# Kernel optimization log

Measured on AMD Instinct MI355X. Metric: run time of the kernel, lower is better.

The kernel has to match this reference:

```python
import jax, jax.numpy as jnp
import numpy as np

EMB, HID, VOCAB, N_SUB = 1024, 2048, 50257, 64
T = N_SUB * 4  # 256 sequential decode steps


def setup_inputs() -> dict:
    key = jax.random.key(0)
    ks = jax.random.split(key, 7)
    s = 0.02  # small init to keep gates out of saturation, like trained weights
    return {
        "emb": jax.random.normal(ks[0], (VOCAB, EMB), jnp.float32) * s,
        "W_ih": jax.random.normal(ks[1], (4 * HID, EMB), jnp.float32) * s,
        "W_hh": jax.random.normal(ks[2], (4 * HID, HID), jnp.float32) * s,
        "b_ih": jax.random.normal(ks[3], (4 * HID,), jnp.float32) * s,
        "b_hh": jax.random.normal(ks[4], (4 * HID,), jnp.float32) * s,
        "W_out": jax.random.normal(ks[5], (VOCAB, HID), jnp.float32) * s,
        "b_out": jax.random.normal(ks[6], (VOCAB,), jnp.float32) * s,
    }


def reference(emb, W_ih, W_hh, b_ih, b_hh, W_out, b_out):
    H = W_hh.shape[1]

    def step(carry, _):
        tok, h, c = carry
        x = emb[tok]  # [EMB] embedding lookup of current token
        # PyTorch LSTM gate order: i, f, g, o
        gates = x @ W_ih.T + b_ih + h @ W_hh.T + b_hh  # [4H]
        i, f, g, o = jnp.split(gates, 4)
        i = jax.nn.sigmoid(i)
        f = jax.nn.sigmoid(f)
        g = jnp.tanh(g)
        o = jax.nn.sigmoid(o)
        c = f * c + i * g
        h = o * jnp.tanh(c)
        logits = h @ W_out.T + b_out  # [VOCAB]
        tok = jnp.argmax(logits).astype(jnp.int32)  # greedy feedback
        return (tok, h, c), logits

    init = (jnp.int32(0), jnp.zeros((H,), emb.dtype), jnp.zeros((H,), emb.dtype))
    _, logits = jax.lax.scan(step, init, None, length=T)
    return logits  # [T, VOCAB] == torch.cat(tokens, 0).squeeze()
```

## Files before the change

### kernel.cpp

```cpp
#include <hip/hip_runtime.h>

#define EMB    1024
#define HID    2048
#define VOCAB  50257
#define T      256
#define NB_LOG 1024
#define NB_GAT (HID / 4)
#define NB_CVT 2048

#define NEG_INF (-3.402823466e38f)


__global__ void k_init(float* __restrict__ ws) {
    int i = blockIdx.x * blockDim.x + threadIdx.x;
    if (i < 3 * HID) ws[i] = 0.0f;
}

__device__ __forceinline__ ushort f2bf(float f) {
    uint32_t u = __float_as_uint(f);
    u += 0x7FFFu + ((u >> 16) & 1u);
    return (ushort)(u >> 16);
}

__global__ __launch_bounds__(256) void k_cvt(const float* __restrict__ src,
                                             ushort* __restrict__ dst, int n4) {
    const int stride = gridDim.x * blockDim.x;
    for (int i = blockIdx.x * blockDim.x + threadIdx.x; i < n4; i += stride) {
        float4 v = ((const float4*)src)[i];
        ushort4 o;
        o.x = f2bf(v.x); o.y = f2bf(v.y); o.z = f2bf(v.z); o.w = f2bf(v.w);
        ((ushort4*)dst)[i] = o;
    }
}

__global__ __launch_bounds__(256) void k_gates(
    const float* __restrict__ emb,
    const float* __restrict__ W_ih, const float* __restrict__ W_hh,
    const float* __restrict__ b_ih, const float* __restrict__ b_hh,
    const float* __restrict__ h_in, float* __restrict__ h_out,
    float* __restrict__ c,
    const float* __restrict__ bmax, const int* __restrict__ bidx,
    int step)
{
    __shared__ float xs[EMB];
    __shared__ float hs[HID];
    __shared__ float redv[4];
    __shared__ int   redi[4];
    __shared__ int   tok_s;

    const int tid  = threadIdx.x;
    const int wave = tid >> 6;
    const int lane = tid & 63;

    if (step == 0) {
        if (tid == 0) tok_s = 0;
    } else {
        float bv = NEG_INF; int bi = 0x7fffffff;
        for (int i = tid; i < NB_LOG; i += 256) {
            float v = bmax[i]; int ix = bidx[i];
            if (v > bv || (v == bv && ix < bi)) { bv = v; bi = ix; }
        }
        for (int off = 32; off; off >>= 1) {
            float ov = __shfl_down(bv, off);
            int   oi = __shfl_down(bi, off);
            if (ov > bv || (ov == bv && oi < bi)) { bv = ov; bi = oi; }
        }
        if (lane == 0) { redv[wave] = bv; redi[wave] = bi; }
        __syncthreads();
        if (tid == 0) {
            for (int w = 1; w < 4; ++w)
                if (redv[w] > bv || (redv[w] == bv && redi[w] < bi)) { bv = redv[w]; bi = redi[w]; }
            tok_s = bi;
        }
    }
    __syncthreads();
    const int tok = tok_s;

    const float* xrow = emb + (size_t)tok * EMB;
    for (int i = tid; i < EMB; i += 256) xs[i] = xrow[i];
    for (int i = tid; i < HID; i += 256) hs[i] = h_in[i];
    __syncthreads();

    const int j = blockIdx.x * 4 + wave;
    float gv[4];
    #pragma unroll
    for (int g = 0; g < 4; ++g) {
        const int row = g * HID + j;
        const float* wi = W_ih + (size_t)row * EMB;
        const float* wh = W_hh + (size_t)row * HID;
        float acc = 0.0f;
        #pragma unroll
        for (int k = lane * 4; k < EMB; k += 256) {
            float4 w4 = *(const float4*)(wi + k);
            float4 x4 = *(const float4*)(xs + k);
            acc += w4.x * x4.x + w4.y * x4.y + w4.z * x4.z + w4.w * x4.w;
        }
        #pragma unroll
        for (int k = lane * 4; k < HID; k += 256) {
            float4 w4 = *(const float4*)(wh + k);
            float4 h4 = *(const float4*)(hs + k);
            acc += w4.x * h4.x + w4.y * h4.y + w4.z * h4.z + w4.w * h4.w;
        }
        for (int off = 32; off; off >>= 1) acc += __shfl_down(acc, off);
        gv[g] = acc;
    }

    if (lane == 0) {
        float gi = gv[0] + b_ih[j]           + b_hh[j];
        float gf = gv[1] + b_ih[HID + j]     + b_hh[HID + j];
        float gg = gv[2] + b_ih[2 * HID + j] + b_hh[2 * HID + j];
        float go = gv[3] + b_ih[3 * HID + j] + b_hh[3 * HID + j];
        float iv = 1.0f / (1.0f + expf(-gi));
        float fv = 1.0f / (1.0f + expf(-gf));
        float gvv = tanhf(gg);
        float ov = 1.0f / (1.0f + expf(-go));
        float cn = fv * c[j] + iv * gvv;
        c[j] = cn;
        h_out[j] = ov * tanhf(cn);
    }
}

__global__ __launch_bounds__(256) void k_logits_bf16(
    const ushort* __restrict__ Wb, const float* __restrict__ b_out,
    const float* __restrict__ h, float* __restrict__ out,
    float* __restrict__ bmax, int* __restrict__ bidx, int step)
{
    __shared__ float hs[HID];
    __shared__ float redv[4];
    __shared__ int   redi[4];

    const int tid  = threadIdx.x;
    const int wave = tid >> 6;
    const int lane = tid & 63;

    for (int i = tid; i < HID; i += 256) hs[i] = h[i];
    __syncthreads();

    float* orow = out + (size_t)step * VOCAB;
    float bv = NEG_INF; int bi = 0x7fffffff;

    for (int r = blockIdx.x * 4 + wave; r < VOCAB; r += NB_LOG * 4) {
        const ushort* w = Wb + (size_t)r * HID;
        float acc = 0.0f;
        #pragma unroll
        for (int k = lane * 4; k < HID; k += 256) {
            uint2 wv = *(const uint2*)(w + k);
            float4 h4 = *(const float4*)(hs + k);
            float w0 = __uint_as_float(wv.x << 16);
            float w1 = __uint_as_float(wv.x & 0xFFFF0000u);
            float w2 = __uint_as_float(wv.y << 16);
            float w3 = __uint_as_float(wv.y & 0xFFFF0000u);
            acc += w0 * h4.x + w1 * h4.y + w2 * h4.z + w3 * h4.w;
        }
        for (int off = 32; off; off >>= 1) acc += __shfl_down(acc, off);
        if (lane == 0) {
            float v = acc + b_out[r];
            orow[r] = v;
            if (v > bv) { bv = v; bi = r; }
        }
    }

    if (lane == 0) { redv[wave] = bv; redi[wave] = bi; }
    __syncthreads();
    if (tid == 0) {
        for (int w = 1; w < 4; ++w)
            if (redv[w] > bv || (redv[w] == bv && redi[w] < bi)) { bv = redv[w]; bi = redi[w]; }
        bmax[blockIdx.x] = bv;
        bidx[blockIdx.x] = bi;
    }
}

__global__ __launch_bounds__(256) void k_logits(
    const float* __restrict__ W_out, const float* __restrict__ b_out,
    const float* __restrict__ h, float* __restrict__ out,
    float* __restrict__ bmax, int* __restrict__ bidx, int step)
{
    __shared__ float hs[HID];
    __shared__ float redv[4];
    __shared__ int   redi[4];

    const int tid  = threadIdx.x;
    const int wave = tid >> 6;
    const int lane = tid & 63;

    for (int i = tid; i < HID; i += 256) hs[i] = h[i];
    __syncthreads();

    float* orow = out + (size_t)step * VOCAB;
    float bv = NEG_INF; int bi = 0x7fffffff;

    for (int r = blockIdx.x * 4 + wave; r < VOCAB; r += NB_LOG * 4) {
        const float* w = W_out + (size_t)r * HID;
        float acc = 0.0f;
        #pragma unroll
        for (int k = lane * 4; k < HID; k += 256) {
            float4 w4 = *(const float4*)(w + k);
            float4 h4 = *(const float4*)(hs + k);
            acc += w4.x * h4.x + w4.y * h4.y + w4.z * h4.z + w4.w * h4.w;
        }
        for (int off = 32; off; off >>= 1) acc += __shfl_down(acc, off);
        if (lane == 0) {
            float v = acc + b_out[r];
            orow[r] = v;
            if (v > bv) { bv = v; bi = r; }
        }
    }

    if (lane == 0) { redv[wave] = bv; redi[wave] = bi; }
    __syncthreads();
    if (tid == 0) {
        for (int w = 1; w < 4; ++w)
            if (redv[w] > bv || (redv[w] == bv && redi[w] < bi)) { bv = redv[w]; bi = redi[w]; }
        bmax[blockIdx.x] = bv;
        bidx[blockIdx.x] = bi;
    }
}

extern "C" void kernel_launch(void* const* d_in, const int* in_sizes, int n_in,
                              void* d_out, int out_size, void* d_ws, size_t ws_size,
                              hipStream_t stream) {
    const float* emb   = (const float*)d_in[0];
    const float* W_ih  = (const float*)d_in[1];
    const float* W_hh  = (const float*)d_in[2];
    const float* b_ih  = (const float*)d_in[3];
    const float* b_hh  = (const float*)d_in[4];
    const float* W_out = (const float*)d_in[5];
    const float* b_out = (const float*)d_in[6];
    float* out = (float*)d_out;

    float* ws   = (float*)d_ws;
    float* hA   = ws;
    float* hB   = ws + HID;
    float* c    = ws + 2 * HID;
    float* bmax = ws + 3 * HID;
    int*   bidx = (int*)(ws + 3 * HID + NB_LOG);
    ushort* Wb  = (ushort*)(ws + 8192);

    const size_t n_wout  = (size_t)VOCAB * HID;
    const size_t ws_need = 8192 * sizeof(float) + n_wout * sizeof(ushort);
    const bool use_bf16  = (ws_size >= ws_need);

    k_init<<<(3 * HID + 255) / 256, 256, 0, stream>>>(ws);
    if (use_bf16) {
        k_cvt<<<NB_CVT, 256, 0, stream>>>(W_out, Wb, (int)(n_wout / 4));
    }

    for (int t = 0; t < T; ++t) {
        float* h_in  = (t & 1) ? hB : hA;
        float* h_out = (t & 1) ? hA : hB;
        k_gates<<<NB_GAT, 256, 0, stream>>>(emb, W_ih, W_hh, b_ih, b_hh,
                                            h_in, h_out, c, bmax, bidx, t);
        if (use_bf16) {
            k_logits_bf16<<<NB_LOG, 256, 0, stream>>>(Wb, b_out, h_out, out, bmax, bidx, t);
        } else {
            k_logits<<<NB_LOG, 256, 0, stream>>>(W_out, b_out, h_out, out, bmax, bidx, t);
        }
    }
}
```

Baseline: 15.94 ms.

## Convert LSTM gate weights to bf16, remap gate blocks, widen logits loads

Adds a tier that converts W_ih and W_hh to bf16 in the workspace once, then runs a new gates kernel that reads the bf16 weights. The gates kernel is restructured so each block computes one hidden unit, with one wave per gate and a shared-memory combine, over 2048 blocks. The logits kernel grid doubles and its inner loop now loads 16-byte vectors of 8 bf16 values. The intent is to halve weight traffic for the recurrent matmuls and raise parallelism, at the cost of bf16 rounding in the gate computation, which could flip argmax tokens, plus the extra conversion kernels.

```diff
diff --git a/kernel.cpp b/kernel.cpp
--- a/kernel.cpp
+++ b/kernel.cpp
@@ -4,8 +4,8 @@
 #define HID    2048
 #define VOCAB  50257
 #define T      256
-#define NB_LOG 1024
-#define NB_GAT (HID / 4)
+#define NB_LOG 2048
+#define NB_GAT 2048
 #define NB_CVT 2048
 
 #define NEG_INF (-3.402823466e38f)
@@ -33,7 +33,117 @@
     }
 }
 
-__global__ __launch_bounds__(256) void k_gates(
+__device__ __forceinline__ int resolve_tok(
+    const float* __restrict__ bmax, const int* __restrict__ bidx,
+    int step, int tid, int wave, int lane,
+    float* redv, int* redi, int* tok_s)
+{
+    if (step == 0) {
+        if (tid == 0) *tok_s = 0;
+    } else {
+        float bv = NEG_INF; int bi = 0x7fffffff;
+        for (int i = tid; i < NB_LOG; i += 256) {
+            float v = bmax[i]; int ix = bidx[i];
+            if (v > bv || (v == bv && ix < bi)) { bv = v; bi = ix; }
+        }
+        for (int off = 32; off; off >>= 1) {
+            float ov = __shfl_down(bv, off);
+            int   oi = __shfl_down(bi, off);
+            if (ov > bv || (ov == bv && oi < bi)) { bv = ov; bi = oi; }
+        }
+        if (lane == 0) { redv[wave] = bv; redi[wave] = bi; }
+        __syncthreads();
+        if (tid == 0) {
+            for (int w = 1; w < 4; ++w)
+                if (redv[w] > bv || (redv[w] == bv && redi[w] < bi)) { bv = redv[w]; bi = redi[w]; }
+            *tok_s = bi;
+        }
+    }
+    __syncthreads();
+    return *tok_s;
+}
+
+__global__ __launch_bounds__(256) void k_gates_bf16(
+    const float* __restrict__ emb,
+    const ushort* __restrict__ Wi, const ushort* __restrict__ Wh,
+    const float* __restrict__ b_ih, const float* __restrict__ b_hh,
+    const float* __restrict__ h_in, float* __restrict__ h_out,
+    float* __restrict__ c,
+    const float* __restrict__ bmax, const int* __restrict__ bidx,
+    int step)
+{
+    __shared__ float xs[EMB];
+    __shared__ float hs[HID];
+    __shared__ float gvs[4];
+    __shared__ float redv[4];
+    __shared__ int   redi[4];
+    __shared__ int   tok_s;
+
+    const int tid  = threadIdx.x;
+    const int wave = tid >> 6;
+    const int lane = tid & 63;
+
+    const int tok = resolve_tok(bmax, bidx, step, tid, wave, lane, redv, redi, &tok_s);
+
+    const float* xrow = emb + (size_t)tok * EMB;
+    for (int i = tid; i < EMB; i += 256) xs[i] = xrow[i];
+    for (int i = tid; i < HID; i += 256) hs[i] = h_in[i];
+    __syncthreads();
+
+    const int j   = blockIdx.x;
+    const int row = wave * HID + j;
+    const ushort* wi = Wi + (size_t)row * EMB;
+    const ushort* wh = Wh + (size_t)row * HID;
+
+    float acc = 0.0f;
+    #pragma unroll
+    for (int k = lane * 8; k < EMB; k += 512) {
+        uint4  wv = *(const uint4*)(wi + k);
+        float4 a  = *(const float4*)(xs + k);
+        float4 b  = *(const float4*)(xs + k + 4);
+        acc += __uint_as_float(wv.x << 16)          * a.x;
+        acc += __uint_as_float(wv.x & 0xFFFF0000u)  * a.y;
+        acc += __uint_as_float(wv.y << 16)          * a.z;
+        acc += __uint_as_float(wv.y & 0xFFFF0000u)  * a.w;
+        acc += __uint_as_float(wv.z << 16)          * b.x;
+        acc += __uint_as_float(wv.z & 0xFFFF0000u)  * b.y;
+        acc += __uint_as_float(wv.w << 16)          * b.z;
+        acc += __uint_as_float(wv.w & 0xFFFF0000u)  * b.w;
+    }
+    #pragma unroll
+    for (int k = lane * 8; k < HID; k += 512) {
+        uint4  wv = *(const uint4*)(wh + k);
+        float4 a  = *(const float4*)(hs + k);
+        float4 b  = *(const float4*)(hs + k + 4);
+        acc += __uint_as_float(wv.x << 16)          * a.x;
+        acc += __uint_as_float(wv.x & 0xFFFF0000u)  * a.y;
+        acc += __uint_as_float(wv.y << 16)          * a.z;
+        acc += __uint_as_float(wv.y & 0xFFFF0000u)  * a.w;
+        acc += __uint_as_float(wv.z << 16)          * b.x;
+        acc += __uint_as_float(wv.z & 0xFFFF0000u)  * b.y;
+        acc += __uint_as_float(wv.w << 16)          * b.z;
+        acc += __uint_as_float(wv.w & 0xFFFF0000u)  * b.w;
+    }
+    for (int off = 32; off; off >>= 1) acc += __shfl_down(acc, off);
+    if (lane == 0) gvs[wave] = acc;
+    __syncthreads();
+
+    if (tid == 0) {
+        float gi = gvs[0] + b_ih[j]           + b_hh[j];
+        float gf = gvs[1] + b_ih[HID + j]     + b_hh[HID + j];
+        float gg = gvs[2] + b_ih[2 * HID + j] + b_hh[2 * HID + j];
+        float go = gvs[3] + b_ih[3 * HID + j] + b_hh[3 * HID + j];
+        float iv = 1.0f / (1.0f + expf(-gi));
+        float fv = 1.0f / (1.0f + expf(-gf));
+        float gvv = tanhf(gg);
+        float ov = 1.0f / (1.0f + expf(-go));
+        float cn = fv * c[j] + iv * gvv;
+        c[j] = cn;
+        h_out[j] = ov * tanhf(cn);
+    }
+}
+
+__global__ __launch_bounds__(256) void k_gates_f32(
     const float* __restrict__ emb,
     const float* __restrict__ W_ih, const float* __restrict__ W_hh,
     const float* __restrict__ b_ih, const float* __restrict__ b_hh,
@@ -44,6 +154,7 @@
 {
     __shared__ float xs[EMB];
     __shared__ float hs[HID];
+    __shared__ float gvs[4];
     __shared__ float redv[4];
     __shared__ int   redi[4];
     __shared__ int   tok_s;
@@ -52,64 +163,40 @@
     const int wave = tid >> 6;
     const int lane = tid & 63;
 
-    if (step == 0) {
-        if (tid == 0) tok_s = 0;
-    } else {
-        float bv = NEG_INF; int bi = 0x7fffffff;
-        for (int i = tid; i < NB_LOG; i += 256) {
-            float v = bmax[i]; int ix = bidx[i];
-            if (v > bv || (v == bv && ix < bi)) { bv = v; bi = ix; }
-        }
-        for (int off = 32; off; off >>= 1) {
-            float ov = __shfl_down(bv, off);
-            int   oi = __shfl_down(bi, off);
-            if (ov > bv || (ov == bv && oi < bi)) { bv = ov; bi = oi; }
-        }
-        if (lane == 0) { redv[wave] = bv; redi[wave] = bi; }
-        __syncthreads();
-        if (tid == 0) {
-            for (int w = 1; w < 4; ++w)
-                if (redv[w] > bv || (redv[w] == bv && redi[w] < bi)) { bv = redv[w]; bi = redi[w]; }
-            tok_s = bi;
-        }
-    }
-    __syncthreads();
-    const int tok = tok_s;
+    const int tok = resolve_tok(bmax, bidx, step, tid, wave, lane, redv, redi, &tok_s);
 
     const float* xrow = emb + (size_t)tok * EMB;
     for (int i = tid; i < EMB; i += 256) xs[i] = xrow[i];
     for (int i = tid; i < HID; i += 256) hs[i] = h_in[i];
     __syncthreads();
 
-    const int j = blockIdx.x * 4 + wave;
-    float gv[4];
+    const int j   = blockIdx.x;
+    const int row = wave * HID + j;
+    const float* wi = W_ih + (size_t)row * EMB;
+    const float* wh = W_hh + (size_t)row * HID;
+
+    float acc = 0.0f;
     #pragma unroll
-    for (int g = 0; g < 4; ++g) {
-        const int row = g * HID + j;
-        const float* wi = W_ih + (size_t)row * EMB;
-        const float* wh = W_hh + (size_t)row * HID;
-        float acc = 0.0f;
-        #pragma unroll
-        for (int k = lane * 4; k < EMB; k += 256) {
-            float4 w4 = *(const float4*)(wi + k);
-            float4 x4 = *(const float4*)(xs + k);
-            acc += w4.x * x4.x + w4.y * x4.y + w4.z * x4.z + w4.w * x4.w;
-        }
-        #pragma unroll
-        for (int k = lane * 4; k < HID; k += 256) {
-            float4 w4 = *(const float4*)(wh + k);
-            float4 h4 = *(const float4*)(hs + k);
-            acc += w4.x * h4.x + w4.y * h4.y + w4.z * h4.z + w4.w * h4.w;
-        }
-        for (int off = 32; off; off >>= 1) acc += __shfl_down(acc, off);
-        gv[g] = acc;
-    }
-
-    if (lane == 0) {
-        float gi = gv[0] + b_ih[j]           + b_hh[j];
-        float gf = gv[1] + b_ih[HID + j]     + b_hh[HID + j];
-        float gg = gv[2] + b_ih[2 * HID + j] + b_hh[2 * HID + j];
-        float go = gv[3] + b_ih[3 * HID + j] + b_hh[3 * HID + j];
+    for (int k = lane * 4; k < EMB; k += 256) {
+        float4 w4 = *(const float4*)(wi + k);
+        float4 x4 = *(const float4*)(xs + k);
+        acc += w4.x * x4.x + w4.y * x4.y + w4.z * x4.z + w4.w * x4.w;
+    }
+    #pragma unroll
+    for (int k = lane * 4; k < HID; k += 256) {
+        float4 w4 = *(const float4*)(wh + k);
+        float4 h4 = *(const float4*)(hs + k);
+        acc += w4.x * h4.x + w4.y * h4.y + w4.z * h4.z + w4.w * h4.w;
+    }
+    for (int off = 32; off; off >>= 1) acc += __shfl_down(acc, off);
+    if (lane == 0) gvs[wave] = acc;
+    __syncthreads();
+
+    if (tid == 0) {
+        float gi = gvs[0] + b_ih[j]           + b_hh[j];
+        float gf = gvs[1] + b_ih[HID + j]     + b_hh[HID + j];
+        float gg = gvs[2] + b_ih[2 * HID + j] + b_hh[2 * HID + j];
+        float go = gvs[3] + b_ih[3 * HID + j] + b_hh[3 * HID + j];
         float iv = 1.0f / (1.0f + expf(-gi));
         float fv = 1.0f / (1.0f + expf(-gf));
         float gvv = tanhf(gg);
@@ -143,14 +230,18 @@
         const ushort* w = Wb + (size_t)r * HID;
         float acc = 0.0f;
         #pragma unroll
-        for (int k = lane * 4; k < HID; k += 256) {
-            uint2 wv = *(const uint2*)(w + k);
-            float4 h4 = *(const float4*)(hs + k);
-            float w0 = __uint_as_float(wv.x << 16);
-            float w1 = __uint_as_float(wv.x & 0xFFFF0000u);
-            float w2 = __uint_as_float(wv.y << 16);
-            float w3 = __uint_as_float(wv.y & 0xFFFF0000u);
-            acc += w0 * h4.x + w1 * h4.y + w2 * h4.z + w3 * h4.w;
+        for (int k = lane * 8; k < HID; k += 512) {
+            uint4  wv = *(const uint4*)(w + k);
+            float4 a  = *(const float4*)(hs + k);
+            float4 b  = *(const float4*)(hs + k + 4);
+            acc += __uint_as_float(wv.x << 16)          * a.x;
+            acc += __uint_as_float(wv.x & 0xFFFF0000u)  * a.y;
+            acc += __uint_as_float(wv.y << 16)          * a.z;
+            acc += __uint_as_float(wv.y & 0xFFFF0000u)  * a.w;
+            acc += __uint_as_float(wv.z << 16)          * b.x;
+            acc += __uint_as_float(wv.z & 0xFFFF0000u)  * b.y;
+            acc += __uint_as_float(wv.w << 16)          * b.z;
+            acc += __uint_as_float(wv.w & 0xFFFF0000u)  * b.w;
         }
         for (int off = 32; off; off >>= 1) acc += __shfl_down(acc, off);
         if (lane == 0) {
@@ -170,7 +261,7 @@
     }
 }
 
-__global__ __launch_bounds__(256) void k_logits(
+__global__ __launch_bounds__(256) void k_logits_f32(
     const float* __restrict__ W_out, const float* __restrict__ b_out,
     const float* __restrict__ h, float* __restrict__ out,
     float* __restrict__ bmax, int* __restrict__ bidx, int step)
@@ -234,26 +325,47 @@
     float* c    = ws + 2 * HID;
     float* bmax = ws + 3 * HID;
     int*   bidx = (int*)(ws + 3 * HID + NB_LOG);
-    ushort* Wb  = (ushort*)(ws + 8192);
-
-    const size_t n_wout  = (size_t)VOCAB * HID;
-    const size_t ws_need = 8192 * sizeof(float) + n_wout * sizeof(ushort);
-    const bool use_bf16  = (ws_size >= ws_need);
+
+    const size_t n_wout = (size_t)VOCAB * HID;
+    const size_t n_wih  = (size_t)4 * HID * EMB;
+    const size_t n_whh  = (size_t)4 * HID * HID;
+
+    const size_t f_wout = 16384;
+    const size_t f_wih  = f_wout + n_wout / 2;
+    const size_t f_whh  = f_wih  + n_wih  / 2;
+    const size_t f_end  = f_whh  + n_whh  / 2;
+
+    const size_t need_part = f_wih * sizeof(float);
+    const size_t need_full = f_end * sizeof(float);
+
+    ushort* Wb_out = (ushort*)(ws + f_wout);
+    ushort* Wb_ih  = (ushort*)(ws + f_wih);
+    ushort* Wb_hh  = (ushort*)(ws + f_whh);
+
+    const int tier = (ws_size >= need_full) ? 2 : (ws_size >= need_part) ? 1 : 0;
 
     k_init<<<(3 * HID + 255) / 256, 256, 0, stream>>>(ws);
-    if (use_bf16) {
-        k_cvt<<<NB_CVT, 256, 0, stream>>>(W_out, Wb, (int)(n_wout / 4));
+    if (tier >= 1)
+        k_cvt<<<NB_CVT, 256, 0, stream>>>(W_out, Wb_out, (int)(n_wout / 4));
+    if (tier == 2) {
+        k_cvt<<<NB_CVT, 256, 0, stream>>>(W_ih, Wb_ih, (int)(n_wih / 4));
+        k_cvt<<<NB_CVT, 256, 0, stream>>>(W_hh, Wb_hh, (int)(n_whh / 4));
     }
 
     for (int t = 0; t < T; ++t) {
         float* h_in  = (t & 1) ? hB : hA;
         float* h_out = (t & 1) ? hA : hB;
-        k_gates<<<NB_GAT, 256, 0, stream>>>(emb, W_ih, W_hh, b_ih, b_hh,
-                                            h_in, h_out, c, bmax, bidx, t);
-        if (use_bf16) {
-            k_logits_bf16<<<NB_LOG, 256, 0, stream>>>(Wb, b_out, h_out, out, bmax, bidx, t);
+        if (tier == 2) {
+            k_gates_bf16<<<NB_GAT, 256, 0, stream>>>(emb, Wb_ih, Wb_hh, b_ih, b_hh,
+                                                     h_in, h_out, c, bmax, bidx, t);
         } else {
-            k_logits<<<NB_LOG, 256, 0, stream>>>(W_out, b_out, h_out, out, bmax, bidx, t);
-        }
-    }
-}
+            k_gates_f32<<<NB_GAT, 256, 0, stream>>>(emb, W_ih, W_hh, b_ih, b_hh,
+                                                    h_in, h_out, c, bmax, bidx, t);
+        }
+        if (tier >= 1) {
+            k_logits_bf16<<<NB_LOG, 256, 0, stream>>>(Wb_out, b_out, h_out, out, bmax, bidx, t);
+        } else {
+            k_logits_f32<<<NB_LOG, 256, 0, stream>>>(W_out, b_out, h_out, out, bmax, bidx, t);
+        }
+    }
+}
```

Result: faster. 14.54 ms (-8.8%).
